# Optimization experiments

Measured on AMD Instinct MI355X. Metric: run time of the kernel, lower is better.

Reference implementation:

```python
import jax, jax.numpy as jnp
import numpy as np

N_E = 8192
E_DIM = 512
N_TOK = 32768
EPS = 1e-10


def setup_inputs() -> dict:
    key = jax.random.key(0)
    k1, k2 = jax.random.split(key)
    z = jax.random.normal(k1, (N_TOK, E_DIM), dtype=jnp.float32)
    weight = jax.random.normal(k2, (N_E, E_DIM), dtype=jnp.float32)
    return {"z": z, "weight": weight}


def reference(z, weight):
    # d[n,k] = ||z_n||^2 + ||e_k||^2 - 2 z_n . e_k  -> [N, n_e]
    d = (jnp.sum(z ** 2, axis=1, keepdims=True)
         + jnp.sum(weight ** 2, axis=1)
         - 2.0 * jnp.matmul(z, weight.T))
    idx = jnp.argmin(d, axis=1)                      # [N]
    # gather instead of one-hot matmul (same math)
    z_q = jnp.take(weight, idx, axis=0)              # [N, e_dim]
    # straight-through estimator
    z_q = z + jax.lax.stop_gradient(z_q - z)
    # e_mean = mean of one-hot encodings = normalized histogram of idx
    counts = jnp.zeros((N_E,), dtype=z.dtype).at[idx].add(1.0)
    e_mean = counts / z.shape[0]
    perplexity = jnp.exp(-jnp.sum(e_mean * jnp.log(e_mean + EPS)))
    return (z_q, perplexity)
```

## Files before the change

kernel.cpp:

```cpp
#include <hip/hip_runtime.h>
#include <stdint.h>


#define NTOK 32768
#define NE   8192
#define DIM  512
#define MARGIN 16.0f

typedef __attribute__((ext_vector_type(8))) int   v8i;
typedef __attribute__((ext_vector_type(4))) float f32x4;

#define SBAR   __builtin_amdgcn_s_barrier()
#define SCHED0 __builtin_amdgcn_sched_barrier(0)
#define SCALE1 0x7F7F7F7F

__device__ __forceinline__ void gl_lds16(const void* g, void* l) {
  __builtin_amdgcn_global_load_lds(
      (const __attribute__((address_space(1))) void*)g,
      (__attribute__((address_space(3))) void*)l, 16, 0, 0);
}

__device__ __forceinline__ int pk8(float a, float b, float c, float d) {
  int r = __builtin_amdgcn_cvt_pk_fp8_f32(a, b, 0, false);
  return __builtin_amdgcn_cvt_pk_fp8_f32(c, d, r, true);
}

__global__ void k_prep_z(const float* __restrict__ z, int2* __restrict__ zb) {
  int i = blockIdx.x * 256 + threadIdx.x;
  const float4* zp = (const float4*)z + (size_t)i * 2;
  float4 a = zp[0], b = zp[1];
  int2 o;
  o.x = pk8(-2.f * a.x, -2.f * a.y, -2.f * a.z, -2.f * a.w);
  o.y = pk8(-2.f * b.x, -2.f * b.y, -2.f * b.z, -2.f * b.w);
  zb[i] = o;
}

__global__ void k_prep_w(const float* __restrict__ w, int2* __restrict__ wb,
                         float* __restrict__ cnorm) {
  int row  = blockIdx.x * 4 + (threadIdx.x >> 6);
  int lane = threadIdx.x & 63;
  const float4* wp = (const float4*)(w + (size_t)row * DIM) + lane * 2;
  float4 a = wp[0], b = wp[1];
  int2 o;
  o.x = pk8(a.x, a.y, a.z, a.w);
  o.y = pk8(b.x, b.y, b.z, b.w);
  wb[(size_t)row * 64 + lane] = o;
  float s = a.x * a.x + a.y * a.y + a.z * a.z + a.w * a.w
          + b.x * b.x + b.y * b.y + b.z * b.z + b.w * b.w;
#pragma unroll
  for (int m = 1; m < 64; m <<= 1) s += __shfl_xor(s, m);
  if (lane == 0) cnorm[row] = s;
}

__global__ void __launch_bounds__(256) k_phase1(
    const unsigned char* __restrict__ zb, const unsigned char* __restrict__ wb,
    const float* __restrict__ cnorm, float* __restrict__ slot2,
    float* __restrict__ slot3) {
  __shared__ char S[2][32768];

  const int tid  = threadIdx.x;
  const int lane = tid & 63;
  const int wv   = tid >> 6;
  const int wr   = wv >> 1;
  const int wc   = wv & 1;
  const int swzb  = (blockIdx.x & 7) * 128 + (blockIdx.x >> 3);
  const int split = swzb >> 8;
  const int tb    = swzb & 255;
  const int l15  = lane & 15;

  const int srcsw = (((lane & 3) ^ ((lane >> 3) & 3)) << 4);
  const unsigned char* zsA = zb + (size_t)(tb * 128 + wv * 32 + (lane >> 2)) * 512 + srcsw;
  const unsigned char* zsB = wb + (size_t)(split * 2048 + wv * 32 + (lane >> 2)) * 512 + srcsw;

  const int g    = lane >> 4;
  const int key  = (lane >> 1) & 3;
  const int offs0 = (g >> 1) * 8192 + (((2 * (g & 1)) ^ key) << 4);
  const int offs1 = (g >> 1) * 8192 + (((2 * (g & 1) + 1) ^ key) << 4);
  int arow[4], brow[4];
#pragma unroll
  for (int i = 0; i < 4; ++i) {
    arow[i] = (wr * 64 + i * 16 + l15) * 64;
    brow[i] = 16384 + (wc * 64 + i * 16 + l15) * 64;
  }

  const float BIG = 3.0e38f;
  float m1s[4][4], m2s[4][4], m3s[4][4];
#pragma unroll
  for (int mi = 0; mi < 4; ++mi)
#pragma unroll
    for (int r = 0; r < 4; ++r) { m1s[mi][r] = BIG; m2s[mi][r] = BIG; m3s[mi][r] = BIG; }

  const unsigned int KMASK = 0xFFFFE000u;

  auto stage = [&](int gg) {
    const int kc = gg & 3, ct2 = gg >> 2;
    char* base = S[gg & 1];
    const unsigned char* ga = zsA + kc * 128;
    char* da = base + wv * 2048;
    gl_lds16(ga,             da);
    gl_lds16(ga + 64,        da + 8192);
    gl_lds16(ga + 8192,      da + 1024);
    gl_lds16(ga + 8192 + 64, da + 8192 + 1024);
    const unsigned char* gb = zsB + ct2 * 65536 + kc * 128;
    char* db = base + 16384 + wv * 2048;
    gl_lds16(gb,             db);
    gl_lds16(gb + 64,        db + 8192);
    gl_lds16(gb + 8192,      db + 1024);
    gl_lds16(gb + 8192 + 64, db + 8192 + 1024);
  };

  stage(0);
  __syncthreads();

  for (int ct = 0; ct < 16; ++ct) {
    const int codebase = split * 2048 + ct * 128 + wc * 64 + l15;
    float cf0 = cnorm[codebase + 0];
    float cf1 = cnorm[codebase + 16];
    float cf2 = cnorm[codebase + 32];
    float cf3 = cnorm[codebase + 48];
    f32x4 acc[4][4];

#pragma unroll 1
    for (int kc = 0; kc < 4; ++kc) {
      const int gg = ct * 4 + kc;
      if (gg < 63) { stage(gg + 1); asm volatile("s_waitcnt vmcnt(8)" ::: "memory"); }
      else         { asm volatile("s_waitcnt vmcnt(0)" ::: "memory"); }
      SBAR; SCHED0;
      const char* P = S[gg & 1];
      v8i a[4], b[4];
#pragma unroll
      for (int i = 0; i < 4; ++i) {
        int4 alo = *(const int4*)(P + arow[i] + offs0);
        int4 ahi = *(const int4*)(P + arow[i] + offs1);
        v8i av; av[0]=alo.x; av[1]=alo.y; av[2]=alo.z; av[3]=alo.w;
        av[4]=ahi.x; av[5]=ahi.y; av[6]=ahi.z; av[7]=ahi.w;
        a[i] = av;
        int4 blo = *(const int4*)(P + brow[i] + offs0);
        int4 bhi = *(const int4*)(P + brow[i] + offs1);
        v8i bv; bv[0]=blo.x; bv[1]=blo.y; bv[2]=blo.z; bv[3]=blo.w;
        bv[4]=bhi.x; bv[5]=bhi.y; bv[6]=bhi.z; bv[7]=bhi.w;
        b[i] = bv;
      }
      __builtin_amdgcn_s_setprio(1);
      if (kc == 0) {
        f32x4 c0 = {cf0, cf0, cf0, cf0}, c1 = {cf1, cf1, cf1, cf1};
        f32x4 c2 = {cf2, cf2, cf2, cf2}, c3 = {cf3, cf3, cf3, cf3};
#pragma unroll
        for (int mi = 0; mi < 4; ++mi) {
          acc[mi][0] = __builtin_amdgcn_mfma_scale_f32_16x16x128_f8f6f4(a[mi], b[0], c0, 0, 0, 0, SCALE1, 0, SCALE1);
          acc[mi][1] = __builtin_amdgcn_mfma_scale_f32_16x16x128_f8f6f4(a[mi], b[1], c1, 0, 0, 0, SCALE1, 0, SCALE1);
          acc[mi][2] = __builtin_amdgcn_mfma_scale_f32_16x16x128_f8f6f4(a[mi], b[2], c2, 0, 0, 0, SCALE1, 0, SCALE1);
          acc[mi][3] = __builtin_amdgcn_mfma_scale_f32_16x16x128_f8f6f4(a[mi], b[3], c3, 0, 0, 0, SCALE1, 0, SCALE1);
        }
      } else {
#pragma unroll
        for (int mi = 0; mi < 4; ++mi)
#pragma unroll
          for (int fj = 0; fj < 4; ++fj)
            acc[mi][fj] = __builtin_amdgcn_mfma_scale_f32_16x16x128_f8f6f4(a[mi], b[fj], acc[mi][fj], 0, 0, 0, SCALE1, 0, SCALE1);
      }
      __builtin_amdgcn_s_setprio(0);
      SBAR;
    }

#pragma unroll
    for (int mi = 0; mi < 4; ++mi) {
#pragma unroll
      for (int r = 0; r < 4; ++r) {
        float M1 = m1s[mi][r], M2 = m2s[mi][r], M3 = m3s[mi][r];
#pragma unroll
        for (int fj = 0; fj < 4; ++fj) {
          float kf = __uint_as_float((__float_as_uint(acc[mi][fj][r]) & KMASK) |
                                     (unsigned)(codebase + fj * 16));
          float t3 = fminf(M3, fmaxf(M2, kf));
          float t2 = fminf(M2, fmaxf(M1, kf));
          M1 = fminf(M1, kf); M2 = t2; M3 = t3;
        }
        m1s[mi][r] = M1; m2s[mi][r] = M2; m3s[mi][r] = M3;
      }
    }
  }

  const int cell = split * 32 + wc * 16 + l15;
#pragma unroll
  for (int mi = 0; mi < 4; ++mi) {
#pragma unroll
    for (int r = 0; r < 4; ++r) {
      int token = tb * 128 + wr * 64 + mi * 16 + (lane >> 4) * 4 + r;
      ((float2*)(slot2 + (size_t)token * 256))[cell] = make_float2(m1s[mi][r], m2s[mi][r]);
      slot3[(size_t)token * 128 + cell] = m3s[mi][r];
    }
  }
}

__global__ void k_select(const float* __restrict__ slot2, const float* __restrict__ slot3,
                         const float* __restrict__ z, const float* __restrict__ w,
                         unsigned int* __restrict__ counts, float* __restrict__ out) {
  const int lane = threadIdx.x & 63;
  const int t = blockIdx.x * 4 + (threadIdx.x >> 6);

  float4 e = *(const float4*)(slot2 + (size_t)t * 256 + lane * 4);
  float2 q = *(const float2*)(slot3 + (size_t)t * 128 + lane * 2);
  float pk = fminf(e.x, e.z);
#pragma unroll
  for (int m = 1; m < 64; m <<= 1) pk = fminf(pk, __shfl_xor(pk, m));
  const unsigned int mb = __float_as_uint(pk);
  int best = (int)(mb & 0x1FFFu);
  const float thr = __uint_as_float(mb & 0xFFFFE000u) + MARGIN;

  const unsigned int KM = 0xFFFFE000u;
  bool c0 = __uint_as_float(__float_as_uint(e.x) & KM) < thr;
  bool c1 = __uint_as_float(__float_as_uint(e.y) & KM) < thr;
  bool c2 = __uint_as_float(__float_as_uint(e.z) & KM) < thr;
  bool c3 = __uint_as_float(__float_as_uint(e.w) & KM) < thr;
  bool h0 = __uint_as_float(__float_as_uint(q.x) & KM) < thr;
  bool h1 = __uint_as_float(__float_as_uint(q.y) & KM) < thr;
  unsigned long long B0 = __ballot(c0), B1 = __ballot(c1);
  unsigned long long B2 = __ballot(c2), B3 = __ballot(c3);
  unsigned long long H0 = __ballot(h0), H1 = __ballot(h1);
  int nc = __popcll(B0) + __popcll(B1) + __popcll(B2) + __popcll(B3);

  if (nc > 1) {
    const float4* zp = (const float4*)(z + (size_t)t * DIM) + lane * 2;
    float4 za = zp[0], zc = zp[1];
    double bestd = 1e300;
    int besti = NE;

    auto eval = [&](int code) {
      const float4* wp = (const float4*)(w + (size_t)code * DIM) + lane * 2;
      float4 wa = wp[0], wv2 = wp[1];
      double d = (double)wa.x * ((double)wa.x - 2.0 * (double)za.x)
               + (double)wa.y * ((double)wa.y - 2.0 * (double)za.y)
               + (double)wa.z * ((double)wa.z - 2.0 * (double)za.z)
               + (double)wa.w * ((double)wa.w - 2.0 * (double)za.w)
               + (double)wv2.x * ((double)wv2.x - 2.0 * (double)zc.x)
               + (double)wv2.y * ((double)wv2.y - 2.0 * (double)zc.y)
               + (double)wv2.z * ((double)wv2.z - 2.0 * (double)zc.z)
               + (double)wv2.w * ((double)wv2.w - 2.0 * (double)zc.w);
#pragma unroll
      for (int m = 1; m < 64; m <<= 1) d += __shfl_xor(d, m);
      if (d < bestd || (d == bestd && code < besti)) { bestd = d; besti = code; }
    };
    auto scan_cell = [&](int cid) {
      int sp = cid >> 5, wcc = (cid >> 4) & 1, col = cid & 15;
      int base = sp * 2048 + wcc * 64 + col;
      for (int ctt = 0; ctt < 16; ++ctt)
        for (int nf = 0; nf < 4; ++nf)
          eval(base + ctt * 128 + nf * 16);
    };

    int i0 = (int)(__float_as_uint(e.x) & 0x1FFFu);
    int i1 = (int)(__float_as_uint(e.y) & 0x1FFFu);
    int i2 = (int)(__float_as_uint(e.z) & 0x1FFFu);
    int i3 = (int)(__float_as_uint(e.w) & 0x1FFFu);
    unsigned long long bm;
    bm = __ballot(c0 && !h0); while (bm) { int s = __ffsll(bm) - 1; bm &= bm - 1; eval(__shfl(i0, s)); }
    bm = __ballot(c1 && !h0); while (bm) { int s = __ffsll(bm) - 1; bm &= bm - 1; eval(__shfl(i1, s)); }
    bm = __ballot(c2 && !h1); while (bm) { int s = __ffsll(bm) - 1; bm &= bm - 1; eval(__shfl(i2, s)); }
    bm = __ballot(c3 && !h1); while (bm) { int s = __ffsll(bm) - 1; bm &= bm - 1; eval(__shfl(i3, s)); }
    bm = H0; while (bm) { int s = __ffsll(bm) - 1; bm &= bm - 1; scan_cell(2 * s); }
    bm = H1; while (bm) { int s = __ffsll(bm) - 1; bm &= bm - 1; scan_cell(2 * s + 1); }
    best = besti;
  }
  if (lane == 0) atomicAdd(&counts[best], 1u);
  const float4* wr4 = (const float4*)(w + (size_t)best * DIM);
  float4* o4 = (float4*)(out + (size_t)t * DIM);
  o4[lane]      = wr4[lane];
  o4[lane + 64] = wr4[lane + 64];
}

__global__ void k_perp(const unsigned int* __restrict__ counts, float* __restrict__ out) {
  __shared__ float red[16];
  float s = 0.f;
  for (int k = threadIdx.x; k < NE; k += 1024) {
    float p = (float)counts[k] * (1.0f / (float)NTOK);
    s += p * logf(p + 1e-10f);
  }
#pragma unroll
  for (int m = 1; m < 64; m <<= 1) s += __shfl_xor(s, m);
  int lane = threadIdx.x & 63, wv = threadIdx.x >> 6;
  if (lane == 0) red[wv] = s;
  __syncthreads();
  if (threadIdx.x == 0) {
    float tot = 0.f;
    for (int i = 0; i < 16; ++i) tot += red[i];
    out[(size_t)NTOK * DIM] = expf(-tot);
  }
}

extern "C" void kernel_launch(void* const* d_in, const int* in_sizes, int n_in,
                              void* d_out, int out_size, void* d_ws, size_t ws_size,
                              hipStream_t stream) {
  const float* z = (const float*)d_in[0];
  const float* w = (const float*)d_in[1];
  float* out = (float*)d_out;
  char* ws = (char*)d_ws;

  unsigned char* zb     = (unsigned char*)(ws);
  float*        slot3   = (float*)(ws + 16777216);
  unsigned char* wb     = (unsigned char*)(ws + 33554432);
  float*        cnorm   = (float*)(ws + 41943040);
  float*        slot2   = (float*)(ws + 41975808);
  unsigned int* counts  = (unsigned int*)(ws + 75661312);

  k_prep_z<<<8192, 256, 0, stream>>>(z, (int2*)zb);
  k_prep_w<<<2048, 256, 0, stream>>>(w, (int2*)wb, cnorm);
  k_phase1<<<1024, 256, 0, stream>>>(zb, wb, cnorm, slot2, slot3);
  hipMemsetAsync(counts, 0, NE * sizeof(unsigned int), stream);
  k_select<<<8192, 256, 0, stream>>>(slot2, slot3, z, w, counts, out);
  k_perp<<<1, 1024, 0, stream>>>(counts, out);
}
```

Baseline: 306.1 us.

## Keep z tile resident in registers and stream only codebook through LDS

The token-side fp8 operand (128 rows x 512 bytes per block) is loaded once from global memory into registers (a_reg[4][4]) instead of being re-staged through LDS for every code tile. LDS then holds only the codebook tiles, halving shared memory per block, and the kernel declares 2 blocks per CU via launch bounds. The kc loop is fully unrolled so the register-resident A operand can be indexed statically. This removes repeated A global->LDS traffic and LDS reads, at the cost of 128 extra VGPRs per thread, which may raise register pressure or cause spills under the occupancy bound.

```diff
diff --git a/kernel.cpp b/kernel.cpp
--- a/kernel.cpp
+++ b/kernel.cpp
@@ -8,6 +8,7 @@
 #define MARGIN 16.0f
 
 typedef __attribute__((ext_vector_type(8))) int   v8i;
+typedef __attribute__((ext_vector_type(4))) int   v4i;
 typedef __attribute__((ext_vector_type(4))) float f32x4;
 
 #define SBAR   __builtin_amdgcn_s_barrier()
@@ -52,11 +53,11 @@
   if (lane == 0) cnorm[row] = s;
 }
 
-__global__ void __launch_bounds__(256) k_phase1(
+__global__ void __launch_bounds__(256, 2) k_phase1(
     const unsigned char* __restrict__ zb, const unsigned char* __restrict__ wb,
     const float* __restrict__ cnorm, float* __restrict__ slot2,
     float* __restrict__ slot3) {
-  __shared__ char S[2][32768];
+  __shared__ char S[2][16384];
 
   const int tid  = threadIdx.x;
   const int lane = tid & 63;
@@ -68,20 +69,28 @@
   const int tb    = swzb & 255;
   const int l15  = lane & 15;
 
+  const unsigned char* aSrc = zb + (size_t)(tb * 128 + wr * 64 + l15) * 512 + ((lane >> 4) << 5);
+  v8i a_reg[4][4];
+#pragma unroll
+  for (int kc = 0; kc < 4; ++kc)
+#pragma unroll
+    for (int mi = 0; mi < 4; ++mi) {
+      const unsigned char* ap = aSrc + mi * 8192 + kc * 128;
+      v4i lo = *(const v4i*)ap;
+      v4i hi = *(const v4i*)(ap + 16);
+      a_reg[kc][mi] = __builtin_shufflevector(lo, hi, 0, 1, 2, 3, 4, 5, 6, 7);
+    }
+
   const int srcsw = (((lane & 3) ^ ((lane >> 3) & 3)) << 4);
-  const unsigned char* zsA = zb + (size_t)(tb * 128 + wv * 32 + (lane >> 2)) * 512 + srcsw;
   const unsigned char* zsB = wb + (size_t)(split * 2048 + wv * 32 + (lane >> 2)) * 512 + srcsw;
 
   const int g    = lane >> 4;
   const int key  = (lane >> 1) & 3;
   const int offs0 = (g >> 1) * 8192 + (((2 * (g & 1)) ^ key) << 4);
   const int offs1 = (g >> 1) * 8192 + (((2 * (g & 1) + 1) ^ key) << 4);
-  int arow[4], brow[4];
-#pragma unroll
-  for (int i = 0; i < 4; ++i) {
-    arow[i] = (wr * 64 + i * 16 + l15) * 64;
-    brow[i] = 16384 + (wc * 64 + i * 16 + l15) * 64;
-  }
+  int brow[4];
+#pragma unroll
+  for (int i = 0; i < 4; ++i) brow[i] = (wc * 64 + i * 16 + l15) * 64;
 
   const float BIG = 3.0e38f;
   float m1s[4][4], m2s[4][4], m3s[4][4];
@@ -94,15 +103,8 @@
 
   auto stage = [&](int gg) {
     const int kc = gg & 3, ct2 = gg >> 2;
-    char* base = S[gg & 1];
-    const unsigned char* ga = zsA + kc * 128;
-    char* da = base + wv * 2048;
-    gl_lds16(ga,             da);
-    gl_lds16(ga + 64,        da + 8192);
-    gl_lds16(ga + 8192,      da + 1024);
-    gl_lds16(ga + 8192 + 64, da + 8192 + 1024);
+    char* db = S[gg & 1] + wv * 2048;
     const unsigned char* gb = zsB + ct2 * 65536 + kc * 128;
-    char* db = base + 16384 + wv * 2048;
     gl_lds16(gb,             db);
     gl_lds16(gb + 64,        db + 8192);
     gl_lds16(gb + 8192,      db + 1024);
@@ -120,26 +122,19 @@
     float cf3 = cnorm[codebase + 48];
     f32x4 acc[4][4];
 
-#pragma unroll 1
+#pragma unroll
     for (int kc = 0; kc < 4; ++kc) {
       const int gg = ct * 4 + kc;
-      if (gg < 63) { stage(gg + 1); asm volatile("s_waitcnt vmcnt(8)" ::: "memory"); }
+      if (gg < 63) { stage(gg + 1); asm volatile("s_waitcnt vmcnt(4)" ::: "memory"); }
       else         { asm volatile("s_waitcnt vmcnt(0)" ::: "memory"); }
       SBAR; SCHED0;
       const char* P = S[gg & 1];
-      v8i a[4], b[4];
+      v8i b[4];
 #pragma unroll
       for (int i = 0; i < 4; ++i) {
-        int4 alo = *(const int4*)(P + arow[i] + offs0);
-        int4 ahi = *(const int4*)(P + arow[i] + offs1);
-        v8i av; av[0]=alo.x; av[1]=alo.y; av[2]=alo.z; av[3]=alo.w;
-        av[4]=ahi.x; av[5]=ahi.y; av[6]=ahi.z; av[7]=ahi.w;
-        a[i] = av;
-        int4 blo = *(const int4*)(P + brow[i] + offs0);
-        int4 bhi = *(const int4*)(P + brow[i] + offs1);
-        v8i bv; bv[0]=blo.x; bv[1]=blo.y; bv[2]=blo.z; bv[3]=blo.w;
-        bv[4]=bhi.x; bv[5]=bhi.y; bv[6]=bhi.z; bv[7]=bhi.w;
-        b[i] = bv;
+        v4i lo = *(const v4i*)(P + brow[i] + offs0);
+        v4i hi = *(const v4i*)(P + brow[i] + offs1);
+        b[i] = __builtin_shufflevector(lo, hi, 0, 1, 2, 3, 4, 5, 6, 7);
       }
       __builtin_amdgcn_s_setprio(1);
       if (kc == 0) {
@@ -147,17 +142,17 @@
         f32x4 c2 = {cf2, cf2, cf2, cf2}, c3 = {cf3, cf3, cf3, cf3};
 #pragma unroll
         for (int mi = 0; mi < 4; ++mi) {
-          acc[mi][0] = __builtin_amdgcn_mfma_scale_f32_16x16x128_f8f6f4(a[mi], b[0], c0, 0, 0, 0, SCALE1, 0, SCALE1);
-          acc[mi][1] = __builtin_amdgcn_mfma_scale_f32_16x16x128_f8f6f4(a[mi], b[1], c1, 0, 0, 0, SCALE1, 0, SCALE1);
-          acc[mi][2] = __builtin_amdgcn_mfma_scale_f32_16x16x128_f8f6f4(a[mi], b[2], c2, 0, 0, 0, SCALE1, 0, SCALE1);
-          acc[mi][3] = __builtin_amdgcn_mfma_scale_f32_16x16x128_f8f6f4(a[mi], b[3], c3, 0, 0, 0, SCALE1, 0, SCALE1);
+          acc[mi][0] = __builtin_amdgcn_mfma_scale_f32_16x16x128_f8f6f4(a_reg[0][mi], b[0], c0, 0, 0, 0, SCALE1, 0, SCALE1);
+          acc[mi][1] = __builtin_amdgcn_mfma_scale_f32_16x16x128_f8f6f4(a_reg[0][mi], b[1], c1, 0, 0, 0, SCALE1, 0, SCALE1);
+          acc[mi][2] = __builtin_amdgcn_mfma_scale_f32_16x16x128_f8f6f4(a_reg[0][mi], b[2], c2, 0, 0, 0, SCALE1, 0, SCALE1);
+          acc[mi][3] = __builtin_amdgcn_mfma_scale_f32_16x16x128_f8f6f4(a_reg[0][mi], b[3], c3, 0, 0, 0, SCALE1, 0, SCALE1);
         }
       } else {
 #pragma unroll
         for (int mi = 0; mi < 4; ++mi)
 #pragma unroll
           for (int fj = 0; fj < 4; ++fj)
-            acc[mi][fj] = __builtin_amdgcn_mfma_scale_f32_16x16x128_f8f6f4(a[mi], b[fj], acc[mi][fj], 0, 0, 0, SCALE1, 0, SCALE1);
+            acc[mi][fj] = __builtin_amdgcn_mfma_scale_f32_16x16x128_f8f6f4(a_reg[kc][mi], b[fj], acc[mi][fj], 0, 0, 0, SCALE1, 0, SCALE1);
       }
       __builtin_amdgcn_s_setprio(0);
       SBAR;
```

Result: slower. 379.1 us (+23.8%).
